# Performance work log

Measured on AMD Instinct MI355X. Metric: run time of the kernel, lower is better.

## Reference

```python
import jax, jax.numpy as jnp
import numpy as np

N_NODES = 100000
N_EDGES = 1600000
N_LABEL = 100000
IN_C, H1, H2, OUT_C = 128, 128, 64, 64
MLP_H = 64


def _glorot(key, shape):
    fan_in, fan_out = shape[0], shape[1]
    s = jnp.sqrt(6.0 / (fan_in + fan_out))
    return jax.random.uniform(key, shape, jnp.float32, -s, s)


def setup_inputs() -> dict:
    key = jax.random.key(0)
    ks = jax.random.split(key, 12)
    x = jax.random.normal(ks[0], (N_NODES, IN_C), jnp.float32)
    edge_index = jax.random.randint(ks[1], (2, N_EDGES), 0, N_NODES, jnp.int64)
    edge_label_index = jax.random.randint(ks[2], (2, N_LABEL), 0, N_NODES, jnp.int64)
    return {
        "x": x,
        "edge_index": edge_index,
        "edge_label_index": edge_label_index,
        "W1": _glorot(ks[3], (IN_C, H1)), "b1": jnp.zeros((H1,), jnp.float32),
        "W2": _glorot(ks[4], (H1, H2)), "b2": jnp.zeros((H2,), jnp.float32),
        "W3": _glorot(ks[5], (H2, OUT_C)), "b3": jnp.zeros((OUT_C,), jnp.float32),
        "Wl1": _glorot(ks[6], (2 * OUT_C, MLP_H)), "bl1": jnp.zeros((MLP_H,), jnp.float32),
        "Wl2": _glorot(ks[7], (MLP_H, 1)), "bl2": jnp.zeros((1,), jnp.float32),
    }


def reference(x, edge_index, edge_label_index, W1, b1, W2, b2, W3, b3, Wl1, bl1, Wl2, bl2):
    n = x.shape[0]
    # GCNConv: add self-loops once; symmetric deg^{-1/2} normalization.
    loops = jnp.arange(n, dtype=edge_index.dtype)
    src = jnp.concatenate([edge_index[0], loops])  # [E+N]
    dst = jnp.concatenate([edge_index[1], loops])
    deg = jax.ops.segment_sum(jnp.ones_like(dst, dtype=x.dtype), dst, num_segments=n)
    deg_isqrt = jnp.where(deg > 0, jax.lax.rsqrt(jnp.maximum(deg, 1e-12)), 0.0)
    norm = deg_isqrt[src] * deg_isqrt[dst]  # [E+N]

    def conv(h, W, b):
        m = (h @ W)[src] * norm[:, None]          # gather + scale per edge
        return jax.ops.segment_sum(m, dst, num_segments=n) + b  # scatter-add

    z = jax.nn.relu(conv(x, W1, b1))   # dropout is identity at eval
    z = jax.nn.relu(conv(z, W2, b2))
    z = conv(z, W3, b3)                # [N, OUT_C]

    s, d = edge_label_index[0], edge_label_index[1]
    pairs = jnp.concatenate([z[s], z[d]], axis=1)  # [E_label, 2*OUT_C]
    h = jax.nn.relu(pairs @ Wl1 + bl1)
    logits = (h @ Wl2 + bl2)[:, 0]
    return logits
```

## Files before the change

kernel.cpp:

```cpp
#include <hip/hip_runtime.h>


typedef _Float16 half8 __attribute__((ext_vector_type(8)));
typedef float floatx4 __attribute__((ext_vector_type(4)));

#define EPB 8
#define CHUNK (256 * EPB)
#define MAXDEG 64


__global__ __launch_bounds__(256) void k_init(
    int* __restrict__ cnt, int n,
    const float* __restrict__ W1, _Float16* __restrict__ Wf1,
    const float* __restrict__ W2, _Float16* __restrict__ Wf2,
    const float* __restrict__ W3, _Float16* __restrict__ Wf3) {
  int b = blockIdx.x;
  if (b >= 112) {
    int i = (b - 112) * 1024 + threadIdx.x * 4;
    if (i + 3 < n) {
      *(int4*)(cnt + i) = make_int4(0, 0, 0, 0);
    } else {
      for (int j = i; j < n && j < i + 4; ++j) cnt[j] = 0;
    }
    return;
  }
  b -= 112;
  return;
}

__global__ __launch_bounds__(256) void k_init2(
    int* __restrict__ cnt, int n,
    const float* __restrict__ W1, _Float16* __restrict__ Wf1,
    const float* __restrict__ W2, _Float16* __restrict__ Wf2,
    const float* __restrict__ W3, _Float16* __restrict__ Wf3) {
  int b = blockIdx.x;
  if (b >= 112) {
    int i = (b - 112) * 1024 + threadIdx.x * 4;
    if (i + 3 < n) {
      *(int4*)(cnt + i) = make_int4(0, 0, 0, 0);
    } else {
      for (int j = i; j < n && j < i + 4; ++j) cnt[j] = 0;
    }
    return;
  }
  const float* W;
  _Float16* Wf;
  int KC, lc;
  if (b < 64)      { W = W1; Wf = Wf1; KC = 16384; lc = 7; }
  else if (b < 96) { b -= 64; W = W2; Wf = Wf2; KC = 8192; lc = 6; }
  else             { b -= 96; W = W3; Wf = Wf3; KC = 4096; lc = 6; }
  int t = b * 256 + threadIdx.x;
  if (t >= KC) return;
  int C = 1 << lc;
  int c = t & (C - 1), k = t >> lc;
  float a = W[t];
  _Float16 h = (_Float16)a;
  _Float16 l = (_Float16)(a - (float)h);
  int ks = k >> 5, ct = c >> 4;
  int lane = ((k & 31) >> 3) * 16 + (c & 15);
  int j = k & 7;
  int base = ((ks * (C >> 4) + ct) * 2) * 512 + lane * 8 + j;
  Wf[base] = h;
  Wf[base + 512] = l;
}


__global__ __launch_bounds__(256) void k_fill1(const int* __restrict__ ei, int E,
                                               int n, int* __restrict__ cnt,
                                               int* __restrict__ csr) {
  int role = blockIdx.x & 7, chunk = blockIdx.x >> 3;
  int ns = (n + 7) / 8;
  int lo = role * ns, hi = min(n, lo + ns);
  int e0 = chunk * CHUNK + threadIdx.x * 2;
#pragma unroll
  for (int q = 0; q < EPB / 2; ++q) {
    int e = e0 + q * 512;
    if (e + 1 < E) {
      int2 d2 = *(const int2*)(ei + E + e);
      int2 s2 = *(const int2*)(ei + e);
      if (d2.x >= lo && d2.x < hi) {
        int pos = atomicAdd(&cnt[d2.x], 1);
        if (pos < MAXDEG) csr[d2.x * MAXDEG + pos] = s2.x;
      }
      if (d2.y >= lo && d2.y < hi) {
        int pos = atomicAdd(&cnt[d2.y], 1);
        if (pos < MAXDEG) csr[d2.y * MAXDEG + pos] = s2.y;
      }
    } else if (e < E) {
      int d = ei[E + e];
      if (d >= lo && d < hi) {
        int pos = atomicAdd(&cnt[d], 1);
        if (pos < MAXDEG) csr[d * MAXDEG + pos] = ei[e];
      }
    }
  }
}


template <int K, int C>
__global__ __launch_bounds__(256) void k_gemm_mfma(const float* __restrict__ A,
                                                   const _Float16* __restrict__ Wf,
                                                   const int* __restrict__ cnt,
                                                   _Float16* __restrict__ out, int n) {
  constexpr int NK = K / 32, NCT = C / 16;
  constexpr int WH = NK * NCT * 2 * 512;
  __shared__ __align__(16) _Float16 Wl[WH];
  int t = threadIdx.x;
  for (int i = t; i < WH / 8; i += 256)
    ((uint4*)Wl)[i] = ((const uint4*)Wf)[i];
  __syncthreads();

  int lane = t & 63, w = t >> 6;
  int rowbase = blockIdx.x * 128 + w * 32;
  int ar0 = rowbase + (lane & 15);
  int kg = (lane >> 4) * 8;

  floatx4 acc[2][NCT];
#pragma unroll
  for (int g = 0; g < 2; ++g)
#pragma unroll
    for (int ct = 0; ct < NCT; ++ct) acc[g][ct] = (floatx4){0.f, 0.f, 0.f, 0.f};

  for (int ks = 0; ks < NK; ++ks) {
    half8 ah[2], al[2];
#pragma unroll
    for (int g = 0; g < 2; ++g) {
      int row = ar0 + g * 16;
      if (row > n - 1) row = n - 1;
      const float* ap = A + (size_t)row * K + ks * 32 + kg;
      float4 u0 = ((const float4*)ap)[0];
      float4 u1 = ((const float4*)ap)[1];
      float av[8] = {u0.x, u0.y, u0.z, u0.w, u1.x, u1.y, u1.z, u1.w};
#pragma unroll
      for (int q = 0; q < 8; ++q) {
        _Float16 h = (_Float16)av[q];
        ah[g][q] = h;
        al[g][q] = (_Float16)(av[q] - (float)h);
      }
    }
#pragma unroll
    for (int ct = 0; ct < NCT; ++ct) {
      const _Float16* bp = &Wl[((ks * NCT + ct) * 2) * 512 + lane * 8];
      half8 bh = *(const half8*)bp;
      half8 bl = *(const half8*)(bp + 512);
#pragma unroll
      for (int g = 0; g < 2; ++g) {
        acc[g][ct] = __builtin_amdgcn_mfma_f32_16x16x32_f16(ah[g], bh, acc[g][ct], 0, 0, 0);
        acc[g][ct] = __builtin_amdgcn_mfma_f32_16x16x32_f16(ah[g], bl, acc[g][ct], 0, 0, 0);
        acc[g][ct] = __builtin_amdgcn_mfma_f32_16x16x32_f16(al[g], bh, acc[g][ct], 0, 0, 0);
      }
    }
  }
  int drbase = rowbase + (lane >> 4) * 4;
  int col = lane & 15;
#pragma unroll
  for (int g = 0; g < 2; ++g)
#pragma unroll
    for (int r = 0; r < 4; ++r) {
      int row = drbase + g * 16 + r;
      if (row < n) {
        float s = rsqrtf((float)(cnt[row] + 1));
#pragma unroll
        for (int ct = 0; ct < NCT; ++ct)
          out[(size_t)row * C + ct * 16 + col] = (_Float16)(acc[g][ct][r] * s);
      }
    }
}


template <bool RELU>
__global__ __launch_bounds__(256) void k_agg128(const _Float16* __restrict__ xs,
                                                const int* __restrict__ cnt,
                                                const int* __restrict__ csr,
                                                const float* __restrict__ bias,
                                                float* __restrict__ out, int n) {
  int gw = (int)((blockIdx.x * blockDim.x + threadIdx.x) >> 6);
  int lane = threadIdx.x & 63;
  if (gw >= n) return;
  int deg = min(cnt[gw], MAXDEG);
  int e0 = gw * MAXDEG, e1 = e0 + deg;
  int qtr = lane >> 4, sub = lane & 15;
  float acc[8] = {};
  int e = e0 + qtr;
  for (; e + 12 < e1; e += 16) {
    int a = __builtin_nontemporal_load(csr + e);
    int b = __builtin_nontemporal_load(csr + e + 4);
    int c = __builtin_nontemporal_load(csr + e + 8);
    int d = __builtin_nontemporal_load(csr + e + 12);
    half8 va = *(const half8*)&xs[(size_t)a * 128 + 8 * sub];
    half8 vb = *(const half8*)&xs[(size_t)b * 128 + 8 * sub];
    half8 vc = *(const half8*)&xs[(size_t)c * 128 + 8 * sub];
    half8 vd = *(const half8*)&xs[(size_t)d * 128 + 8 * sub];
#pragma unroll
    for (int j = 0; j < 8; ++j)
      acc[j] += (float)va[j] + (float)vb[j] + (float)vc[j] + (float)vd[j];
  }
  for (; e < e1; e += 4) {
    int a = __builtin_nontemporal_load(csr + e);
    half8 va = *(const half8*)&xs[(size_t)a * 128 + 8 * sub];
#pragma unroll
    for (int j = 0; j < 8; ++j) acc[j] += (float)va[j];
  }
#pragma unroll
  for (int j = 0; j < 8; ++j) {
    acc[j] += __shfl_xor(acc[j], 32, 64);
    acc[j] += __shfl_xor(acc[j], 16, 64);
  }
  if (qtr == 0) {
    float qi = rsqrtf((float)(deg + 1));
    half8 self = *(const half8*)&xs[(size_t)gw * 128 + 8 * sub];
#pragma unroll
    for (int j = 0; j < 8; ++j) {
      float r = qi * (acc[j] + (float)self[j]) + bias[8 * sub + j];
      if (RELU) r = fmaxf(r, 0.f);
      out[(size_t)gw * 128 + 8 * sub + j] = r;
    }
  }
}


template <bool RELU>
__global__ __launch_bounds__(256) void k_agg64(const _Float16* __restrict__ xs,
                                               const int* __restrict__ cnt,
                                               const int* __restrict__ csr,
                                               const float* __restrict__ bias,
                                               float* __restrict__ out, int n) {
  int gw = (int)((blockIdx.x * blockDim.x + threadIdx.x) >> 6);
  int lane = threadIdx.x & 63;
  if (gw >= n) return;
  int deg = min(cnt[gw], MAXDEG);
  int e0 = gw * MAXDEG, e1 = e0 + deg;
  int oct = lane >> 3, sub = lane & 7;
  float acc[8] = {};
  int e = e0 + oct;
  for (; e + 8 < e1; e += 16) {
    int a = __builtin_nontemporal_load(csr + e);
    int b = __builtin_nontemporal_load(csr + e + 8);
    half8 va = *(const half8*)&xs[(size_t)a * 64 + 8 * sub];
    half8 vb = *(const half8*)&xs[(size_t)b * 64 + 8 * sub];
#pragma unroll
    for (int j = 0; j < 8; ++j) acc[j] += (float)va[j] + (float)vb[j];
  }
  for (; e < e1; e += 8) {
    int a = __builtin_nontemporal_load(csr + e);
    half8 va = *(const half8*)&xs[(size_t)a * 64 + 8 * sub];
#pragma unroll
    for (int j = 0; j < 8; ++j) acc[j] += (float)va[j];
  }
#pragma unroll
  for (int j = 0; j < 8; ++j) {
    acc[j] += __shfl_xor(acc[j], 32, 64);
    acc[j] += __shfl_xor(acc[j], 16, 64);
    acc[j] += __shfl_xor(acc[j], 8, 64);
  }
  if (oct == 0) {
    float qi = rsqrtf((float)(deg + 1));
    half8 self = *(const half8*)&xs[(size_t)gw * 64 + 8 * sub];
#pragma unroll
    for (int j = 0; j < 8; ++j) {
      float r = qi * (acc[j] + (float)self[j]) + bias[8 * sub + j];
      if (RELU) r = fmaxf(r, 0.f);
      out[(size_t)gw * 64 + 8 * sub + j] = r;
    }
  }
}


__global__ __launch_bounds__(256) void k_mlp(const float* __restrict__ z,
                                             const int* __restrict__ eli, int nlab,
                                             const float* __restrict__ Wl1,
                                             const float* __restrict__ bl1,
                                             const float* __restrict__ Wl2,
                                             const float* __restrict__ bl2,
                                             float* __restrict__ out) {
  constexpr int K = 128, TM = 4, LDA = K + 4;
  __shared__ float Wl[K * 64];
  __shared__ float Al[64 * LDA];
  int t = threadIdx.x;
  for (int i = t; i < K * 64 / 4; i += 256)
    ((float4*)Wl)[i] = ((const float4*)Wl1)[i];
  int rowbase = blockIdx.x * 64;
  {
    int r = t >> 2, p = t & 3;
    int row = rowbase + r;
    int idx = 0;
    if (row < nlab) idx = (p < 2) ? eli[row] : eli[nlab + row];
    const float4* src = (const float4*)(z + (size_t)idx * 64);
    int srcq = (p & 1) * 8;
    int dst = r * LDA + (p >= 2 ? 64 : 0) + (p & 1) * 32;
#pragma unroll
    for (int q = 0; q < 8; ++q)
      *(float4*)&Al[dst + 4 * q] = src[srcq + q];
  }
  __syncthreads();
  int tx = t & 15, ty = t >> 4;
  float acc[TM][4] = {};
  for (int k = 0; k < K; ++k) {
    float a[TM];
#pragma unroll
    for (int i = 0; i < TM; ++i) a[i] = Al[(ty * TM + i) * LDA + k];
    float4 w = *(const float4*)&Wl[k * 64 + tx * 4];
#pragma unroll
    for (int i = 0; i < TM; ++i) {
      acc[i][0] += a[i] * w.x;
      acc[i][1] += a[i] * w.y;
      acc[i][2] += a[i] * w.z;
      acc[i][3] += a[i] * w.w;
    }
  }
  float4 b1v = *(const float4*)&bl1[tx * 4];
  float4 w2v = *(const float4*)&Wl2[tx * 4];
  float bias2 = bl2[0];
  float part[TM];
#pragma unroll
  for (int i = 0; i < TM; ++i) {
    float h0 = fmaxf(acc[i][0] + b1v.x, 0.f);
    float h1 = fmaxf(acc[i][1] + b1v.y, 0.f);
    float h2 = fmaxf(acc[i][2] + b1v.z, 0.f);
    float h3 = fmaxf(acc[i][3] + b1v.w, 0.f);
    part[i] = h0 * w2v.x + h1 * w2v.y + h2 * w2v.z + h3 * w2v.w;
  }
#pragma unroll
  for (int i = 0; i < TM; ++i) {
#pragma unroll
    for (int m = 1; m < 16; m <<= 1)
      part[i] += __shfl_xor(part[i], m, 64);
  }
  if (tx == 0) {
#pragma unroll
    for (int i = 0; i < TM; ++i) {
      int row = rowbase + ty * TM + i;
      if (row < nlab) out[row] = part[i] + bias2;
    }
  }
}


extern "C" void kernel_launch(void* const* d_in, const int* in_sizes, int n_in,
                              void* d_out, int out_size, void* d_ws, size_t ws_size,
                              hipStream_t stream) {
  const float* x   = (const float*)d_in[0];
  const int*   ei  = (const int*)d_in[1];
  const int*   eli = (const int*)d_in[2];
  const float* W1  = (const float*)d_in[3];
  const float* b1  = (const float*)d_in[4];
  const float* W2  = (const float*)d_in[5];
  const float* b2  = (const float*)d_in[6];
  const float* W3  = (const float*)d_in[7];
  const float* b3  = (const float*)d_in[8];
  const float* Wl1 = (const float*)d_in[9];
  const float* bl1 = (const float*)d_in[10];
  const float* Wl2 = (const float*)d_in[11];
  const float* bl2 = (const float*)d_in[12];
  float* out = (float*)d_out;
  const int n    = in_sizes[0] / 128;
  const int E    = in_sizes[1] / 2;
  const int nlab = in_sizes[2] / 2;
  (void)n_in; (void)out_size; (void)ws_size;

  char* ws = (char*)d_ws;
  size_t off = 0;
  auto alloc = [&](size_t bytes) -> void* {
    void* p = ws + off;
    off = (off + bytes + 255) & ~(size_t)255;
    return p;
  };
  float*     bufZ  = (float*)alloc((size_t)n * 128 * 4);
  _Float16*  bufXW = (_Float16*)alloc((size_t)n * 128 * 2);
  int*       csr   = (int*)alloc((size_t)n * MAXDEG * 4);
  int*       cnt   = (int*)alloc((size_t)n * 4);
  _Float16*  Wf1   = (_Float16*)alloc(128 * 128 * 2 * 2);
  _Float16*  Wf2   = (_Float16*)alloc(128 * 64 * 2 * 2);
  _Float16*  Wf3   = (_Float16*)alloc(64 * 64 * 2 * 2);
  float*     z1    = bufZ;
  float*     z2    = bufZ;
  float*     z3    = bufZ + (size_t)n * 64;

  const int CH  = (E + CHUNK - 1) / CHUNK;
  const int HB  = 8 * CH;
  const int GT  = (n + 127) / 128;
  const int ZB  = (n + 1023) / 1024;
  const int aggb = (n + 3) / 4;

  k_init2<<<112 + ZB, 256, 0, stream>>>(cnt, n, W1, Wf1, W2, Wf2, W3, Wf3);
  k_fill1<<<HB, 256, 0, stream>>>(ei, E, n, cnt, csr);

  k_gemm_mfma<128, 128><<<GT, 256, 0, stream>>>(x, Wf1, cnt, bufXW, n);
  k_agg128<true><<<aggb, 256, 0, stream>>>(bufXW, cnt, csr, b1, z1, n);
  k_gemm_mfma<128, 64><<<GT, 256, 0, stream>>>(z1, Wf2, cnt, bufXW, n);
  k_agg64<true><<<aggb, 256, 0, stream>>>(bufXW, cnt, csr, b2, z2, n);
  k_gemm_mfma<64, 64><<<GT, 256, 0, stream>>>(z2, Wf3, cnt, bufXW, n);
  k_agg64<false><<<aggb, 256, 0, stream>>>(bufXW, cnt, csr, b3, z3, n);
  k_mlp<<<(nlab + 63) / 64, 256, 0, stream>>>(z3, eli, nlab, Wl1, bl1, Wl2, bl2, out);
}
```

Baseline: 339.5 us.

## Split GEMM outputs into 16-column slabs and pin aggregation slabs per XCD

The MFMA GEMM now writes its output as contiguous 16-column slabs, each holding n×16 halves, instead of row-major rows. The aggregation kernels assign each slab to blocks with the same blockIdx&7. If blocks are dispatched round-robin across the 8 XCDs, each XCD then gathers from one slab of about 3.2 MB that can stay resident in its L2. For the 64-wide layers, the 4 slabs are paired with two node halves so all 8 roles are used. The trade-offs are that CSR indices are re-read once per role, many more waves are launched, half the edge slots sit idle at typical degree, and the shuffle reductions get longer. An unused init kernel is also deleted.

```diff
diff --git a/kernel.cpp b/kernel.cpp
--- a/kernel.cpp
+++ b/kernel.cpp
@@ -8,25 +8,6 @@
 #define CHUNK (256 * EPB)
 #define MAXDEG 64
 
-
-__global__ __launch_bounds__(256) void k_init(
-    int* __restrict__ cnt, int n,
-    const float* __restrict__ W1, _Float16* __restrict__ Wf1,
-    const float* __restrict__ W2, _Float16* __restrict__ Wf2,
-    const float* __restrict__ W3, _Float16* __restrict__ Wf3) {
-  int b = blockIdx.x;
-  if (b >= 112) {
-    int i = (b - 112) * 1024 + threadIdx.x * 4;
-    if (i + 3 < n) {
-      *(int4*)(cnt + i) = make_int4(0, 0, 0, 0);
-    } else {
-      for (int j = i; j < n && j < i + 4; ++j) cnt[j] = 0;
-    }
-    return;
-  }
-  b -= 112;
-  return;
-}
 
 __global__ __launch_bounds__(256) void k_init2(
     int* __restrict__ cnt, int n,
@@ -162,105 +143,86 @@
         float s = rsqrtf((float)(cnt[row] + 1));
 #pragma unroll
         for (int ct = 0; ct < NCT; ++ct)
-          out[(size_t)row * C + ct * 16 + col] = (_Float16)(acc[g][ct][r] * s);
+          out[((size_t)ct * n + row) * 16 + col] = (_Float16)(acc[g][ct][r] * s);
       }
     }
 }
 
 
 template <bool RELU>
-__global__ __launch_bounds__(256) void k_agg128(const _Float16* __restrict__ xs,
-                                                const int* __restrict__ cnt,
-                                                const int* __restrict__ csr,
-                                                const float* __restrict__ bias,
-                                                float* __restrict__ out, int n) {
-  int gw = (int)((blockIdx.x * blockDim.x + threadIdx.x) >> 6);
+__global__ __launch_bounds__(256) void k_agg128cs(const _Float16* __restrict__ xs,
+                                                  const int* __restrict__ cnt,
+                                                  const int* __restrict__ csr,
+                                                  const float* __restrict__ bias,
+                                                  float* __restrict__ out, int n) {
+  int role = blockIdx.x & 7;
+  int node = (blockIdx.x >> 3) * 4 + (threadIdx.x >> 6);
   int lane = threadIdx.x & 63;
-  if (gw >= n) return;
-  int deg = min(cnt[gw], MAXDEG);
-  int e0 = gw * MAXDEG, e1 = e0 + deg;
-  int qtr = lane >> 4, sub = lane & 15;
+  if (node >= n) return;
+  int deg = min(cnt[node], MAXDEG);
+  const _Float16* tab = xs + (size_t)role * n * 16;
+  int eslot = lane >> 1, half = lane & 1;
+  int e0 = node * MAXDEG;
   float acc[8] = {};
-  int e = e0 + qtr;
-  for (; e + 12 < e1; e += 16) {
-    int a = __builtin_nontemporal_load(csr + e);
-    int b = __builtin_nontemporal_load(csr + e + 4);
-    int c = __builtin_nontemporal_load(csr + e + 8);
-    int d = __builtin_nontemporal_load(csr + e + 12);
-    half8 va = *(const half8*)&xs[(size_t)a * 128 + 8 * sub];
-    half8 vb = *(const half8*)&xs[(size_t)b * 128 + 8 * sub];
-    half8 vc = *(const half8*)&xs[(size_t)c * 128 + 8 * sub];
-    half8 vd = *(const half8*)&xs[(size_t)d * 128 + 8 * sub];
-#pragma unroll
-    for (int j = 0; j < 8; ++j)
-      acc[j] += (float)va[j] + (float)vb[j] + (float)vc[j] + (float)vd[j];
-  }
-  for (; e < e1; e += 4) {
-    int a = __builtin_nontemporal_load(csr + e);
-    half8 va = *(const half8*)&xs[(size_t)a * 128 + 8 * sub];
-#pragma unroll
-    for (int j = 0; j < 8; ++j) acc[j] += (float)va[j];
-  }
-#pragma unroll
-  for (int j = 0; j < 8; ++j) {
-    acc[j] += __shfl_xor(acc[j], 32, 64);
-    acc[j] += __shfl_xor(acc[j], 16, 64);
-  }
-  if (qtr == 0) {
+  for (int e = eslot; e < deg; e += 32) {
+    int a = __builtin_nontemporal_load(csr + e0 + e);
+    half8 v = *(const half8*)&tab[(size_t)a * 16 + 8 * half];
+#pragma unroll
+    for (int j = 0; j < 8; ++j) acc[j] += (float)v[j];
+  }
+#pragma unroll
+  for (int m = 2; m <= 32; m <<= 1)
+#pragma unroll
+    for (int j = 0; j < 8; ++j) acc[j] += __shfl_xor(acc[j], m, 64);
+  if (lane < 2) {
     float qi = rsqrtf((float)(deg + 1));
-    half8 self = *(const half8*)&xs[(size_t)gw * 128 + 8 * sub];
+    half8 self = *(const half8*)&tab[(size_t)node * 16 + 8 * half];
 #pragma unroll
     for (int j = 0; j < 8; ++j) {
-      float r = qi * (acc[j] + (float)self[j]) + bias[8 * sub + j];
+      float r = qi * (acc[j] + (float)self[j]) + bias[role * 16 + 8 * half + j];
       if (RELU) r = fmaxf(r, 0.f);
-      out[(size_t)gw * 128 + 8 * sub + j] = r;
+      out[(size_t)node * 128 + role * 16 + 8 * half + j] = r;
     }
   }
 }
 
 
 template <bool RELU>
-__global__ __launch_bounds__(256) void k_agg64(const _Float16* __restrict__ xs,
-                                               const int* __restrict__ cnt,
-                                               const int* __restrict__ csr,
-                                               const float* __restrict__ bias,
-                                               float* __restrict__ out, int n) {
-  int gw = (int)((blockIdx.x * blockDim.x + threadIdx.x) >> 6);
+__global__ __launch_bounds__(256) void k_agg64cs(const _Float16* __restrict__ xs,
+                                                 const int* __restrict__ cnt,
+                                                 const int* __restrict__ csr,
+                                                 const float* __restrict__ bias,
+                                                 float* __restrict__ out, int n) {
+  int role = blockIdx.x & 7;
+  int cb = role >> 1, nh = role & 1;
+  int half_n = (n + 1) / 2;
+  int nlo = nh * half_n, nhi = min(n, nlo + half_n);
+  int node = nlo + (blockIdx.x >> 3) * 4 + (threadIdx.x >> 6);
   int lane = threadIdx.x & 63;
-  if (gw >= n) return;
-  int deg = min(cnt[gw], MAXDEG);
-  int e0 = gw * MAXDEG, e1 = e0 + deg;
-  int oct = lane >> 3, sub = lane & 7;
+  if (node >= nhi) return;
+  int deg = min(cnt[node], MAXDEG);
+  const _Float16* tab = xs + (size_t)cb * n * 16;
+  int eslot = lane >> 1, half = lane & 1;
+  int e0 = node * MAXDEG;
   float acc[8] = {};
-  int e = e0 + oct;
-  for (; e + 8 < e1; e += 16) {
-    int a = __builtin_nontemporal_load(csr + e);
-    int b = __builtin_nontemporal_load(csr + e + 8);
-    half8 va = *(const half8*)&xs[(size_t)a * 64 + 8 * sub];
-    half8 vb = *(const half8*)&xs[(size_t)b * 64 + 8 * sub];
-#pragma unroll
-    for (int j = 0; j < 8; ++j) acc[j] += (float)va[j] + (float)vb[j];
-  }
-  for (; e < e1; e += 8) {
-    int a = __builtin_nontemporal_load(csr + e);
-    half8 va = *(const half8*)&xs[(size_t)a * 64 + 8 * sub];
-#pragma unroll
-    for (int j = 0; j < 8; ++j) acc[j] += (float)va[j];
-  }
-#pragma unroll
-  for (int j = 0; j < 8; ++j) {
-    acc[j] += __shfl_xor(acc[j], 32, 64);
-    acc[j] += __shfl_xor(acc[j], 16, 64);
-    acc[j] += __shfl_xor(acc[j], 8, 64);
-  }
-  if (oct == 0) {
+  for (int e = eslot; e < deg; e += 32) {
+    int a = __builtin_nontemporal_load(csr + e0 + e);
+    half8 v = *(const half8*)&tab[(size_t)a * 16 + 8 * half];
+#pragma unroll
+    for (int j = 0; j < 8; ++j) acc[j] += (float)v[j];
+  }
+#pragma unroll
+  for (int m = 2; m <= 32; m <<= 1)
+#pragma unroll
+    for (int j = 0; j < 8; ++j) acc[j] += __shfl_xor(acc[j], m, 64);
+  if (lane < 2) {
     float qi = rsqrtf((float)(deg + 1));
-    half8 self = *(const half8*)&xs[(size_t)gw * 64 + 8 * sub];
+    half8 self = *(const half8*)&tab[(size_t)node * 16 + 8 * half];
 #pragma unroll
     for (int j = 0; j < 8; ++j) {
-      float r = qi * (acc[j] + (float)self[j]) + bias[8 * sub + j];
+      float r = qi * (acc[j] + (float)self[j]) + bias[cb * 16 + 8 * half + j];
       if (RELU) r = fmaxf(r, 0.f);
-      out[(size_t)gw * 64 + 8 * sub + j] = r;
+      out[(size_t)node * 64 + cb * 16 + 8 * half + j] = r;
     }
   }
 }
@@ -380,16 +342,17 @@
   const int HB  = 8 * CH;
   const int GT  = (n + 127) / 128;
   const int ZB  = (n + 1023) / 1024;
-  const int aggb = (n + 3) / 4;
+  const int A128 = 8 * ((n + 3) / 4);
+  const int A64  = 8 * (((n + 1) / 2 + 3) / 4);
 
   k_init2<<<112 + ZB, 256, 0, stream>>>(cnt, n, W1, Wf1, W2, Wf2, W3, Wf3);
   k_fill1<<<HB, 256, 0, stream>>>(ei, E, n, cnt, csr);
 
   k_gemm_mfma<128, 128><<<GT, 256, 0, stream>>>(x, Wf1, cnt, bufXW, n);
-  k_agg128<true><<<aggb, 256, 0, stream>>>(bufXW, cnt, csr, b1, z1, n);
+  k_agg128cs<true><<<A128, 256, 0, stream>>>(bufXW, cnt, csr, b1, z1, n);
   k_gemm_mfma<128, 64><<<GT, 256, 0, stream>>>(z1, Wf2, cnt, bufXW, n);
-  k_agg64<true><<<aggb, 256, 0, stream>>>(bufXW, cnt, csr, b2, z2, n);
+  k_agg64cs<true><<<A64, 256, 0, stream>>>(bufXW, cnt, csr, b2, z2, n);
   k_gemm_mfma<64, 64><<<GT, 256, 0, stream>>>(z2, Wf3, cnt, bufXW, n);
-  k_agg64<false><<<aggb, 256, 0, stream>>>(bufXW, cnt, csr, b3, z3, n);
+  k_agg64cs<false><<<A64, 256, 0, stream>>>(bufXW, cnt, csr, b3, z3, n);
   k_mlp<<<(nlab + 63) / 64, 256, 0, stream>>>(z3, eli, nlab, Wl1, bl1, Wl2, bl2, out);
 }
```

Result: slower. 818.3 us (+141.0%).
